# Performance work log

Measured on AMD Instinct MI355X. Metric: run time of the kernel, lower is better.

## Reference

```python
import jax, jax.numpy as jnp
import numpy as np

N = 524288
FEAT = 32
RES = 256
BOUNDS = 1.3

OFFSETS = np.array([[-1.0, 0.0], [-0.5, 0.0], [0.5, 0.0], [1.0, 0.0],
                    [0.0, -1.0], [0.0, -0.5], [0.0, 0.5], [0.0, 1.0],
                    [0.5, 0.5], [0.5, -0.5], [-0.5, 0.5], [-0.5, -0.5]],
                   dtype=np.float32)  # [12, 2]


def setup_inputs() -> dict:
    key = jax.random.key(0)
    k = jax.random.split(key, 7)
    pts = (jax.random.uniform(k[0], (N, 3), jnp.float32) * 2.0 - 1.0) * (BOUNDS * 0.9)
    timestamps = jax.random.uniform(k[1], (N,), jnp.float32)
    scales = jax.random.uniform(k[2], (N, 3), jnp.float32) * 0.05
    plane0 = jax.random.normal(k[3], (FEAT, RES, RES), jnp.float32) * 0.1
    plane1 = jax.random.normal(k[4], (FEAT, RES, RES), jnp.float32) * 0.1
    plane2 = jax.random.normal(k[5], (FEAT, RES, RES), jnp.float32) * 0.1
    aabb = jnp.array([[BOUNDS, BOUNDS, BOUNDS], [-BOUNDS, -BOUNDS, -BOUNDS]], jnp.float32)
    return {"pts": pts, "timestamps": timestamps, "scales": scales,
            "plane0": plane0, "plane1": plane1, "plane2": plane2, "aabb": aabb}


def _bilinear_sample(plane, xy):
    # plane: [C, H, W]; xy: [M, 2] normalized coords in [-1, 1] (x -> W, y -> H)
    C, H, W = plane.shape
    x = jnp.clip((xy[:, 0] + 1.0) * 0.5 * (W - 1), 0.0, W - 1)
    y = jnp.clip((xy[:, 1] + 1.0) * 0.5 * (H - 1), 0.0, H - 1)
    x0 = jnp.floor(x)
    y0 = jnp.floor(y)
    wx = x - x0
    wy = y - y0
    x0i = x0.astype(jnp.int32)
    y0i = y0.astype(jnp.int32)
    x1i = jnp.minimum(x0i + 1, W - 1)
    y1i = jnp.minimum(y0i + 1, H - 1)
    f00 = plane[:, y0i, x0i]  # [C, M]
    f10 = plane[:, y0i, x1i]
    f01 = plane[:, y1i, x0i]
    f11 = plane[:, y1i, x1i]
    out = (f00 * ((1.0 - wx) * (1.0 - wy)) + f10 * (wx * (1.0 - wy))
           + f01 * ((1.0 - wx) * wy) + f11 * (wx * wy))
    return out.T  # [M, C]


def _interpolate_mul(pts_n, scales, planes):
    offsets = jnp.asarray(OFFSETS)  # [12, 2]
    pairs = ((0, 1), (0, 2), (1, 2))
    interp = 1.0
    for i, (q, r) in enumerate(pairs):
        base = pts_n[:, (q, r)]                                   # [N, 2]
        so = scales[:, (q, r)][:, None, :] * offsets[None, :, :]  # [N, 12, 2]
        pts13 = jnp.concatenate([base[:, None, :], base[:, None, :] + so], axis=1)  # [N, 13, 2]
        feat = _bilinear_sample(planes[i], pts13.reshape(-1, 2))  # [N*13, C]
        feat = feat.reshape(-1, 13, feat.shape[-1]).mean(axis=1)  # [N, C]
        interp = interp * feat
    return interp


def reference(pts, timestamps, scales, plane0, plane1, plane2, aabb):
    # normalize_aabb: aabb = [[+b,+b,+b], [-b,-b,-b]]
    pts_n = (pts - aabb[0]) * (2.0 / (aabb[1] - aabb[0])) - 1.0
    pts_n = pts_n.reshape(-1, pts_n.shape[-1])
    del timestamps  # detached / unused in feature interpolation
    return _interpolate_mul(pts_n, scales, (plane0, plane1, plane2))
```

## Files before the change

kernel.cpp:

```cpp
#include <hip/hip_runtime.h>
#include <hip/hip_fp16.h>

#define RES 256
#define FEAT 32
#define PLANE_ELEMS (FEAT * RES * RES)
#define NBINS 32768


__global__ __launch_bounds__(256) void transpose_quant(const float* __restrict__ p0,
                                                       const float* __restrict__ p1,
                                                       const float* __restrict__ p2,
                                                       __half* __restrict__ outp) {
    int t = blockIdx.x * 256 + threadIdx.x;
    int pl = t >> 21;
    int r = t & (PLANE_ELEMS - 1);
    int c = r & 31;
    int x = (r >> 5) & 255;
    int y = r >> 13;
    const float* in = pl == 0 ? p0 : (pl == 1 ? p1 : p2);
    outp[t] = __float2half(in[c * (RES * RES) + y * RES + x]);
}

__device__ inline unsigned spread3(unsigned v) {
    unsigned r = 0;
    r |= (v & 1u);
    r |= (v & 2u) << 2;
    r |= (v & 4u) << 4;
    r |= (v & 8u) << 6;
    r |= (v & 16u) << 8;
    return r;
}

__global__ __launch_bounds__(256) void build_hist_keys(const float* __restrict__ pts,
                                                       const float* __restrict__ aabb,
                                                       int* __restrict__ hist,
                                                       int* __restrict__ keys, int n) {
    int i = blockIdx.x * 256 + threadIdx.x;
    if (i >= n) return;
    float a00 = aabb[0], a01 = aabb[1], a02 = aabb[2];
    float a10 = aabb[3], a11 = aabb[4], a12 = aabb[5];
    float px = (pts[i * 3 + 0] - a00) * (2.0f / (a10 - a00)) - 1.0f;
    float py = (pts[i * 3 + 1] - a01) * (2.0f / (a11 - a01)) - 1.0f;
    float pz = (pts[i * 3 + 2] - a02) * (2.0f / (a12 - a02)) - 1.0f;
    unsigned ux = (unsigned)min(max((int)((px + 1.0f) * 16.0f), 0), 31);
    unsigned uy = (unsigned)min(max((int)((py + 1.0f) * 16.0f), 0), 31);
    unsigned uz = (unsigned)min(max((int)((pz + 1.0f) * 16.0f), 0), 31);
    int key = (int)(spread3(ux) | (spread3(uy) << 1) | (spread3(uz) << 2));
    keys[i] = key;
    atomicAdd(&hist[key], 1);
}

__global__ __launch_bounds__(1024) void scan_hist(int* __restrict__ hist) {
    __shared__ int sums[1024];
    int t = threadIdx.x;
    int base = t * 32;
    int local[32];
    int s = 0;
#pragma unroll
    for (int i = 0; i < 32; ++i) { local[i] = hist[base + i]; s += local[i]; }
    sums[t] = s;
    __syncthreads();
    for (int off = 1; off < 1024; off <<= 1) {
        int v = 0;
        if (t >= off) v = sums[t - off];
        __syncthreads();
        if (t >= off) sums[t] += v;
        __syncthreads();
    }
    int excl = (t == 0) ? 0 : sums[t - 1];
#pragma unroll
    for (int i = 0; i < 32; ++i) { hist[base + i] = excl; excl += local[i]; }
}

__global__ __launch_bounds__(256) void scatter_pack(const float* __restrict__ pts,
                                                    const float* __restrict__ scales,
                                                    const float* __restrict__ aabb,
                                                    const int* __restrict__ keys,
                                                    int* __restrict__ hist,
                                                    float* __restrict__ ppk,
                                                    int* __restrict__ idx_s, int n) {
    int i = blockIdx.x * 256 + threadIdx.x;
    if (i >= n) return;
    float a00 = aabb[0], a01 = aabb[1], a02 = aabb[2];
    float a10 = aabb[3], a11 = aabb[4], a12 = aabb[5];
    float px = (pts[i * 3 + 0] - a00) * (2.0f / (a10 - a00)) - 1.0f;
    float py = (pts[i * 3 + 1] - a01) * (2.0f / (a11 - a01)) - 1.0f;
    float pz = (pts[i * 3 + 2] - a02) * (2.0f / (a12 - a02)) - 1.0f;
    int pos = atomicAdd(&hist[keys[i]], 1);
    float4* o = reinterpret_cast<float4*>(ppk) + (size_t)pos * 2;
    o[0] = make_float4((px + 1.0f) * 127.5f, (py + 1.0f) * 127.5f, (pz + 1.0f) * 127.5f, 0.0f);
    o[1] = make_float4(scales[i * 3 + 0] * 63.75f, scales[i * 3 + 1] * 63.75f,
                       scales[i * 3 + 2] * 63.75f, 0.0f);
    idx_s[pos] = i;
}


__device__ inline void corner_fma(float fs[8], const char* __restrict__ p, float w) {
    float4 raw = *reinterpret_cast<const float4*>(p);
    const __half2* h = reinterpret_cast<const __half2*>(&raw);
#pragma unroll
    for (int c = 0; c < 4; ++c) {
        float2 f = __half22float2(h[c]);
        fs[2 * c]     = fmaf(f.x, w, fs[2 * c]);
        fs[2 * c + 1] = fmaf(f.y, w, fs[2 * c + 1]);
    }
}

__device__ inline void pair_accum(float interp[8], const __half* __restrict__ plane,
                                  float cx, float cy, float hx, float hy, int cg) {
    const int SI[13] = {2, 0, 1, 3, 4, 2, 2, 2, 2, 3, 3, 1, 1};
    const int SJ[13] = {2, 2, 2, 2, 2, 0, 1, 3, 4, 3, 1, 3, 1};

    float wx[5], wxc[5], wy[5], wyc[5];
    int colA[5], colB[5], rowA[5], rowB[5];
    int chan = cg * 16;
#pragma unroll
    for (int k = 0; k < 5; ++k) {
        float x = fminf(fmaxf(cx + (float)(k - 2) * hx, 0.0f), 255.0f);
        float xf = floorf(x);
        int x0 = (int)xf;
        int x1 = min(x0 + 1, 255);
        wx[k] = x - xf; wxc[k] = 1.0f - wx[k];
        colA[k] = x0 * 64 + chan;
        colB[k] = x1 * 64 + chan;
        float y = fminf(fmaxf(cy + (float)(k - 2) * hy, 0.0f), 255.0f);
        float yf = floorf(y);
        int y0 = (int)yf;
        int y1 = min(y0 + 1, 255);
        wy[k] = y - yf; wyc[k] = 1.0f - wy[k];
        rowA[k] = y0 * (RES * 64);
        rowB[k] = y1 * (RES * 64);
    }

    float fs[8] = {0, 0, 0, 0, 0, 0, 0, 0};
    const char* base = reinterpret_cast<const char*>(plane);
#pragma unroll
    for (int s = 0; s < 13; ++s) {
        int i = SI[s], j = SJ[s];
        float w00 = wxc[i] * wyc[j];
        float w10 = wx[i] * wyc[j];
        float w01 = wxc[i] * wy[j];
        float w11 = wx[i] * wy[j];
        corner_fma(fs, base + (rowA[j] + colA[i]), w00);
        corner_fma(fs, base + (rowA[j] + colB[i]), w10);
        corner_fma(fs, base + (rowB[j] + colA[i]), w01);
        corner_fma(fs, base + (rowB[j] + colB[i]), w11);
    }
    const float inv13 = 1.0f / 13.0f;
#pragma unroll
    for (int c = 0; c < 8; ++c) interp[c] *= fs[c] * inv13;
}

__global__ __launch_bounds__(256) void wpf_main4(const float* __restrict__ ppk,
                                                 const int* __restrict__ idx_s,
                                                 const __half* __restrict__ planes,
                                                 float* __restrict__ out, int n, int swizzle) {
    int b = blockIdx.x;
    if (swizzle) {
        int nb = gridDim.x;
        int chunk = nb >> 3;
        b = (b & 7) * chunk + (b >> 3);
    }
    int t = b * 256 + threadIdx.x;
    int pt = t >> 2;
    int cg = t & 3;
    if (pt >= n) return;

    float4 a  = reinterpret_cast<const float4*>(ppk)[(size_t)pt * 2];
    float4 hh = reinterpret_cast<const float4*>(ppk)[(size_t)pt * 2 + 1];

    float interp[8] = {1, 1, 1, 1, 1, 1, 1, 1};
#pragma unroll 1
    for (int pr = 0; pr < 3; ++pr) {
        const __half* pl = planes + (size_t)pr * PLANE_ELEMS;
        float cx = (pr == 2) ? a.y : a.x;
        float cy = (pr == 0) ? a.y : a.z;
        float hx = (pr == 2) ? hh.y : hh.x;
        float hy = (pr == 0) ? hh.y : hh.z;
        pair_accum(interp, pl, cx, cy, hx, hy, cg);
    }

    int oi = idx_s[pt];
    float4* o = reinterpret_cast<float4*>(out + (size_t)oi * 32 + cg * 8);
    o[0] = make_float4(interp[0], interp[1], interp[2], interp[3]);
    o[1] = make_float4(interp[4], interp[5], interp[6], interp[7]);
}

__global__ __launch_bounds__(256) void wpf_plain(const float* __restrict__ pts,
                                                 const float* __restrict__ scales,
                                                 const float* __restrict__ p0,
                                                 const float* __restrict__ p1,
                                                 const float* __restrict__ p2,
                                                 const float* __restrict__ aabb,
                                                 float* __restrict__ out, int n) {
    const float offx[13] = {0.f, -1.f, -0.5f, 0.5f, 1.f, 0.f, 0.f, 0.f, 0.f, 0.5f, 0.5f, -0.5f, -0.5f};
    const float offy[13] = {0.f, 0.f, 0.f, 0.f, 0.f, -1.f, -0.5f, 0.5f, 1.f, 0.5f, -0.5f, 0.5f, -0.5f};
    int t = blockIdx.x * 256 + threadIdx.x;
    int pt = t >> 3;
    int cg = t & 7;
    if (pt >= n) return;
    float a00 = aabb[0], a01 = aabb[1], a02 = aabb[2];
    float a10 = aabb[3], a11 = aabb[4], a12 = aabb[5];
    float px = (pts[pt * 3 + 0] - a00) * (2.0f / (a10 - a00)) - 1.0f;
    float py = (pts[pt * 3 + 1] - a01) * (2.0f / (a11 - a01)) - 1.0f;
    float pz = (pts[pt * 3 + 2] - a02) * (2.0f / (a12 - a02)) - 1.0f;
    float scx = scales[pt * 3 + 0], scy = scales[pt * 3 + 1], scz = scales[pt * 3 + 2];
    float4 interp = make_float4(1.f, 1.f, 1.f, 1.f);
    for (int pair = 0; pair < 3; ++pair) {
        const float* plane = pair == 0 ? p0 : (pair == 1 ? p1 : p2);
        float bx = pair == 2 ? py : px;
        float by = pair == 0 ? py : pz;
        float sx = pair == 2 ? scy : scx;
        float sy = pair == 0 ? scy : scz;
        float4 featsum = make_float4(0.f, 0.f, 0.f, 0.f);
        for (int s = 0; s < 13; ++s) {
            float x = fminf(fmaxf((bx + sx * offx[s] + 1.0f) * 127.5f, 0.0f), 255.0f);
            float y = fminf(fmaxf((by + sy * offy[s] + 1.0f) * 127.5f, 0.0f), 255.0f);
            float x0f = floorf(x), y0f = floorf(y);
            float wx = x - x0f, wy = y - y0f;
            int x0 = (int)x0f, y0 = (int)y0f;
            int x1 = min(x0 + 1, RES - 1), y1 = min(y0 + 1, RES - 1);
            float w00 = (1.0f - wx) * (1.0f - wy), w10 = wx * (1.0f - wy);
            float w01 = (1.0f - wx) * wy, w11 = wx * wy;
            int c0 = cg << 2;
            for (int c = 0; c < 4; ++c) {
                const float* pl = plane + (size_t)(c0 + c) * (RES * RES);
                float f = pl[y0 * RES + x0] * w00 + pl[y0 * RES + x1] * w10 +
                          pl[y1 * RES + x0] * w01 + pl[y1 * RES + x1] * w11;
                (&featsum.x)[c] += f;
            }
        }
        const float inv13 = 1.0f / 13.0f;
        interp.x *= featsum.x * inv13;
        interp.y *= featsum.y * inv13;
        interp.z *= featsum.z * inv13;
        interp.w *= featsum.w * inv13;
    }
    reinterpret_cast<float4*>(out)[(size_t)pt * 8 + cg] = interp;
}

extern "C" void kernel_launch(void* const* d_in, const int* in_sizes, int n_in,
                              void* d_out, int out_size, void* d_ws, size_t ws_size,
                              hipStream_t stream) {
    const float* pts    = (const float*)d_in[0];
    const float* scales = (const float*)d_in[2];
    const float* p0     = (const float*)d_in[3];
    const float* p1     = (const float*)d_in[4];
    const float* p2     = (const float*)d_in[5];
    const float* aabb   = (const float*)d_in[6];
    float* out = (float*)d_out;

    int n = in_sizes[0] / 3;
    int pt_blocks = (n + 255) / 256;

    size_t planes_hbytes = (size_t)3 * PLANE_ELEMS * sizeof(__half);
    size_t ppk_bytes = (size_t)n * 8 * sizeof(float);
    size_t idx_bytes = (size_t)n * sizeof(int);
    size_t key_bytes = (size_t)n * sizeof(int);
    size_t hist_bytes = (size_t)NBINS * sizeof(int);
    size_t need = planes_hbytes + ppk_bytes + idx_bytes + key_bytes + hist_bytes;

    if (ws_size >= need) {
        __half* planes_h = (__half*)d_ws;
        float*  ppk   = (float*)((char*)d_ws + planes_hbytes);
        int*    idx_s = (int*)((char*)ppk + ppk_bytes);
        int*    keys  = idx_s + n;
        int*    hist  = keys + n;

        transpose_quant<<<(3 * PLANE_ELEMS) / 256, 256, 0, stream>>>(p0, p1, p2, planes_h);
        hipMemsetAsync(hist, 0, hist_bytes, stream);
        build_hist_keys<<<pt_blocks, 256, 0, stream>>>(pts, aabb, hist, keys, n);
        scan_hist<<<1, 1024, 0, stream>>>(hist);
        scatter_pack<<<pt_blocks, 256, 0, stream>>>(pts, scales, aabb, keys, hist,
                                                    ppk, idx_s, n);
        int main_blocks = (n * 4 + 255) / 256;
        int swizzle = (main_blocks % 8 == 0) ? 1 : 0;
        wpf_main4<<<main_blocks, 256, 0, stream>>>(ppk, idx_s, planes_h, out, n, swizzle);
    } else {
        int main_blocks = (n * 8 + 255) / 256;
        wpf_plain<<<main_blocks, 256, 0, stream>>>(pts, scales, p0, p1, p2, aabb, out, n);
    }
}
```

Baseline: 374.9 us.

## Use two threads per point with 16 channels each and fma_mix half accumulation

The main sampling kernel now gives each point 2 threads of 16 channels instead of 4 threads of 8 channels. Each corner fetch becomes two 16-byte loads, and the half-to-float conversion plus FMA is merged into v_fma_mix_f32 inline assembly. The transpose/quantize kernel now writes 8 halves per thread as one 16-byte store. The aim is to cut repeated per-point coordinate and weight computation and conversion instructions, at the cost of higher register pressure per thread and fewer threads for hiding gather latency.

Result: slower. 430.8 us (+14.9%).

```diff
diff --git a/kernel.cpp b/kernel.cpp
--- a/kernel.cpp
+++ b/kernel.cpp
@@ -12,13 +12,17 @@
                                                        const float* __restrict__ p2,
                                                        __half* __restrict__ outp) {
     int t = blockIdx.x * 256 + threadIdx.x;
-    int pl = t >> 21;
-    int r = t & (PLANE_ELEMS - 1);
-    int c = r & 31;
-    int x = (r >> 5) & 255;
-    int y = r >> 13;
-    const float* in = pl == 0 ? p0 : (pl == 1 ? p1 : p2);
-    outp[t] = __float2half(in[c * (RES * RES) + y * RES + x]);
+    int pl = t >> 18;
+    int r = t & 262143;
+    int cg = r & 3;
+    int x = (r >> 2) & 255;
+    int y = r >> 10;
+    const float* in = (pl == 0 ? p0 : (pl == 1 ? p1 : p2)) + y * 256 + x;
+    union { __half h[8]; uint4 v; } u;
+#pragma unroll
+    for (int k = 0; k < 8; ++k)
+        u.h[k] = __float2half(in[(size_t)(cg * 8 + k) * 65536]);
+    reinterpret_cast<uint4*>(outp)[((size_t)pl << 18) | ((size_t)((y << 8) | x) << 2) | cg] = u.v;
 }
 
 __device__ inline unsigned spread3(unsigned v) {
@@ -95,63 +99,64 @@
 }
 
 
-__device__ inline void corner_fma(float fs[8], const char* __restrict__ p, float w) {
-    float4 raw = *reinterpret_cast<const float4*>(p);
-    const __half2* h = reinterpret_cast<const __half2*>(&raw);
-#pragma unroll
-    for (int c = 0; c < 4; ++c) {
-        float2 f = __half22float2(h[c]);
-        fs[2 * c]     = fmaf(f.x, w, fs[2 * c]);
-        fs[2 * c + 1] = fmaf(f.y, w, fs[2 * c + 1]);
-    }
-}
-
-__device__ inline void pair_accum(float interp[8], const __half* __restrict__ plane,
-                                  float cx, float cy, float hx, float hy, int cg) {
+__device__ __forceinline__ void corner16(float fs[16], const char* __restrict__ p, float w) {
+    uint4 r0 = *reinterpret_cast<const uint4*>(p);
+    uint4 r1 = *reinterpret_cast<const uint4*>(p + 16);
+    unsigned u[8] = {r0.x, r0.y, r0.z, r0.w, r1.x, r1.y, r1.z, r1.w};
+#pragma unroll
+    for (int i = 0; i < 8; ++i) {
+        asm("v_fma_mix_f32 %0, %1, %2, %0 op_sel_hi:[1,0,0]"
+            : "+v"(fs[2 * i]) : "v"(u[i]), "v"(w));
+        asm("v_fma_mix_f32 %0, %1, %2, %0 op_sel:[1,0,0] op_sel_hi:[1,0,0]"
+            : "+v"(fs[2 * i + 1]) : "v"(u[i]), "v"(w));
+    }
+}
+
+__device__ __forceinline__ void pair_accum16(float interp[16], const __half* __restrict__ plane,
+                                             float cx, float cy, float hx, float hy, int chan) {
     const int SI[13] = {2, 0, 1, 3, 4, 2, 2, 2, 2, 3, 3, 1, 1};
     const int SJ[13] = {2, 2, 2, 2, 2, 0, 1, 3, 4, 3, 1, 3, 1};
 
-    float wx[5], wxc[5], wy[5], wyc[5];
+    float wx[5], wy[5];
     int colA[5], colB[5], rowA[5], rowB[5];
-    int chan = cg * 16;
+    float hx2 = hx + hx, hy2 = hy + hy;
+    float xs[5] = {cx - hx2, cx - hx, cx, cx + hx, cx + hx2};
+    float ys[5] = {cy - hy2, cy - hy, cy, cy + hy, cy + hy2};
+    int colMax = 255 * 64 + chan;
 #pragma unroll
     for (int k = 0; k < 5; ++k) {
-        float x = fminf(fmaxf(cx + (float)(k - 2) * hx, 0.0f), 255.0f);
+        float x = fminf(fmaxf(xs[k], 0.0f), 255.0f);
         float xf = floorf(x);
-        int x0 = (int)xf;
-        int x1 = min(x0 + 1, 255);
-        wx[k] = x - xf; wxc[k] = 1.0f - wx[k];
-        colA[k] = x0 * 64 + chan;
-        colB[k] = x1 * 64 + chan;
-        float y = fminf(fmaxf(cy + (float)(k - 2) * hy, 0.0f), 255.0f);
+        wx[k] = x - xf;
+        colA[k] = (int)xf * 64 + chan;
+        colB[k] = min(colA[k] + 64, colMax);
+        float y = fminf(fmaxf(ys[k], 0.0f), 255.0f);
         float yf = floorf(y);
-        int y0 = (int)yf;
-        int y1 = min(y0 + 1, 255);
-        wy[k] = y - yf; wyc[k] = 1.0f - wy[k];
-        rowA[k] = y0 * (RES * 64);
-        rowB[k] = y1 * (RES * 64);
-    }
-
-    float fs[8] = {0, 0, 0, 0, 0, 0, 0, 0};
+        wy[k] = y - yf;
+        rowA[k] = (int)yf * (RES * 64);
+        rowB[k] = min(rowA[k] + RES * 64, 255 * RES * 64);
+    }
+
+    float fs[16];
+#pragma unroll
+    for (int c = 0; c < 16; ++c) fs[c] = 0.0f;
     const char* base = reinterpret_cast<const char*>(plane);
 #pragma unroll
     for (int s = 0; s < 13; ++s) {
         int i = SI[s], j = SJ[s];
-        float w00 = wxc[i] * wyc[j];
-        float w10 = wx[i] * wyc[j];
-        float w01 = wxc[i] * wy[j];
-        float w11 = wx[i] * wy[j];
-        corner_fma(fs, base + (rowA[j] + colA[i]), w00);
-        corner_fma(fs, base + (rowA[j] + colB[i]), w10);
-        corner_fma(fs, base + (rowB[j] + colA[i]), w01);
-        corner_fma(fs, base + (rowB[j] + colB[i]), w11);
+        float wxi = wx[i], wyj = wy[j];
+        float wxc = 1.0f - wxi, wyc = 1.0f - wyj;
+        corner16(fs, base + (rowA[j] + colA[i]), wxc * wyc);
+        corner16(fs, base + (rowA[j] + colB[i]), wxi * wyc);
+        corner16(fs, base + (rowB[j] + colA[i]), wxc * wyj);
+        corner16(fs, base + (rowB[j] + colB[i]), wxi * wyj);
     }
     const float inv13 = 1.0f / 13.0f;
 #pragma unroll
-    for (int c = 0; c < 8; ++c) interp[c] *= fs[c] * inv13;
-}
-
-__global__ __launch_bounds__(256) void wpf_main4(const float* __restrict__ ppk,
+    for (int c = 0; c < 16; ++c) interp[c] *= fs[c] * inv13;
+}
+
+__global__ __launch_bounds__(256) void wpf_main2(const float* __restrict__ ppk,
                                                  const int* __restrict__ idx_s,
                                                  const __half* __restrict__ planes,
                                                  float* __restrict__ out, int n, int swizzle) {
@@ -162,14 +167,18 @@
         b = (b & 7) * chunk + (b >> 3);
     }
     int t = b * 256 + threadIdx.x;
-    int pt = t >> 2;
-    int cg = t & 3;
+    int pt = t >> 1;
+    int cg = t & 1;
     if (pt >= n) return;
 
     float4 a  = reinterpret_cast<const float4*>(ppk)[(size_t)pt * 2];
     float4 hh = reinterpret_cast<const float4*>(ppk)[(size_t)pt * 2 + 1];
-
-    float interp[8] = {1, 1, 1, 1, 1, 1, 1, 1};
+    int chan = cg * 32;
+
+    float interp[16];
+#pragma unroll
+    for (int c = 0; c < 16; ++c) interp[c] = 1.0f;
+
 #pragma unroll 1
     for (int pr = 0; pr < 3; ++pr) {
         const __half* pl = planes + (size_t)pr * PLANE_ELEMS;
@@ -177,13 +186,15 @@
         float cy = (pr == 0) ? a.y : a.z;
         float hx = (pr == 2) ? hh.y : hh.x;
         float hy = (pr == 0) ? hh.y : hh.z;
-        pair_accum(interp, pl, cx, cy, hx, hy, cg);
+        pair_accum16(interp, pl, cx, cy, hx, hy, chan);
     }
 
     int oi = idx_s[pt];
-    float4* o = reinterpret_cast<float4*>(out + (size_t)oi * 32 + cg * 8);
+    float4* o = reinterpret_cast<float4*>(out + (size_t)oi * 32 + cg * 16);
     o[0] = make_float4(interp[0], interp[1], interp[2], interp[3]);
     o[1] = make_float4(interp[4], interp[5], interp[6], interp[7]);
+    o[2] = make_float4(interp[8], interp[9], interp[10], interp[11]);
+    o[3] = make_float4(interp[12], interp[13], interp[14], interp[15]);
 }
 
 __global__ __launch_bounds__(256) void wpf_plain(const float* __restrict__ pts,
@@ -267,15 +278,15 @@
         int*    keys  = idx_s + n;
         int*    hist  = keys + n;
 
-        transpose_quant<<<(3 * PLANE_ELEMS) / 256, 256, 0, stream>>>(p0, p1, p2, planes_h);
+        transpose_quant<<<(3 * 262144) / 256, 256, 0, stream>>>(p0, p1, p2, planes_h);
         hipMemsetAsync(hist, 0, hist_bytes, stream);
         build_hist_keys<<<pt_blocks, 256, 0, stream>>>(pts, aabb, hist, keys, n);
         scan_hist<<<1, 1024, 0, stream>>>(hist);
         scatter_pack<<<pt_blocks, 256, 0, stream>>>(pts, scales, aabb, keys, hist,
                                                     ppk, idx_s, n);
-        int main_blocks = (n * 4 + 255) / 256;
+        int main_blocks = (n * 2 + 255) / 256;
         int swizzle = (main_blocks % 8 == 0) ? 1 : 0;
-        wpf_main4<<<main_blocks, 256, 0, stream>>>(ppk, idx_s, planes_h, out, n, swizzle);
+        wpf_main2<<<main_blocks, 256, 0, stream>>>(ppk, idx_s, planes_h, out, n, swizzle);
     } else {
         int main_blocks = (n * 8 + 255) / 256;
         wpf_plain<<<main_blocks, 256, 0, stream>>>(pts, scales, p0, p1, p2, aabb, out, n);
```
